# Performance work log

Measured on AMD Instinct MI355X. Metric: run time of the kernel, lower is better.

The kernel has to match this reference:

```python
import jax, jax.numpy as jnp
import numpy as np

N = 50000      # nodes
DEG = 16       # in-degree per node -> E = 800k edges
IN = 256       # in_size
HID = 32       # hid_size
HEAD = 4       # heads in first layer
OUT = 40       # out_size (classes)
HH = HID * HEAD  # 128, hidden width
NEG_SLOPE = 0.2


def setup_inputs() -> dict:
    key = jax.random.key(0)
    ks = jax.random.split(key, 16)
    E = N * DEG
    src = jax.random.randint(ks[0], (E,), 0, N)
    dst = jnp.repeat(jnp.arange(N), DEG)  # every node has DEG in-edges

    def nrm(k, shape):
        return jax.random.normal(k, shape, jnp.float32) * 0.1

    return dict(
        features=jax.random.normal(ks[1], (N, IN), jnp.float32),
        src=src, dst=dst,
        # layer 1: GATConv(IN -> HID, HEAD heads)
        W1=nrm(ks[2], (IN, HH)), al1=nrm(ks[3], (HEAD, HID)), ar1=nrm(ks[4], (HEAD, HID)), b1=nrm(ks[5], (HH,)),
        # hidden layer: GATConv(HH -> HH, 1 head)
        Wh=nrm(ks[6], (HH, HH)), alh=nrm(ks[7], (1, HH)), arh=nrm(ks[8], (1, HH)), bh=nrm(ks[9], (HH,)),
        # layer 2: GATConv(HH -> OUT, 1 head)
        W2=nrm(ks[10], (HH, OUT)), al2=nrm(ks[11], (1, OUT)), ar2=nrm(ks[12], (1, OUT)), b2=nrm(ks[13], (OUT,)),
    )


def gat_conv(x, src, dst, W, al, ar, b):
    """DGL-style GATConv. x:[N,F], W:[F,H*D], al/ar:[H,D], b:[H*D]. Returns [N,H,D]."""
    n = x.shape[0]
    H, D = al.shape
    feat = (x @ W).reshape(n, H, D)                 # [N,H,D]
    el = jnp.sum(feat * al, axis=-1)                # [N,H]
    er = jnp.sum(feat * ar, axis=-1)                # [N,H]
    e = jax.nn.leaky_relu(el[src] + er[dst], NEG_SLOPE)  # [E,H] per-edge logits
    # segment softmax over each destination's in-edges
    emax = jax.lax.stop_gradient(jax.ops.segment_max(e, dst, num_segments=n))  # [N,H]
    ex = jnp.exp(e - emax[dst])                     # [E,H]
    den = jax.ops.segment_sum(ex, dst, num_segments=n)  # [N,H]
    alpha = ex / den[dst]                           # [E,H]
    out = jax.ops.segment_sum(feat[src] * alpha[:, :, None], dst, num_segments=n)  # [N,H,D]
    return out + b.reshape(1, H, D)


def reference(features, src, dst, W1, al1, ar1, b1, Wh, alh, arh, bh, W2, al2, ar2, b2):
    # conv1 -> flatten heads -> relu
    h = jax.nn.relu(gat_conv(features, src, dst, W1, al1, ar1, b1).reshape(N, HH))
    # hidden GATConv (1 head) -> mean over head -> relu (dropout is identity in eval)
    h = jax.nn.relu(gat_conv(h, src, dst, Wh, alh, arh, bh).mean(axis=1))
    # conv2 (1 head) -> mean over head -> log_softmax
    h = gat_conv(h, src, dst, W2, al2, ar2, b2).mean(axis=1)
    return jax.nn.log_softmax(h, axis=1)
```

## Files before the change

### kernel.cpp

```cpp
#include <hip/hip_runtime.h>
#include <cstddef>
#include <math.h>

#define NN 50000
#define DEG 16
#define NEG_SLOPE 0.2f

typedef __attribute__((ext_vector_type(8))) short bf16x8;
typedef __attribute__((ext_vector_type(4))) float f32x4;

__device__ inline unsigned short f2bf(float x) {
    unsigned u = __float_as_uint(x);
    return (unsigned short)((u + 0x7FFF + ((u >> 16) & 1)) >> 16);
}
__device__ inline float bf2f(unsigned short u) {
    return __uint_as_float(((unsigned)u) << 16);
}
__device__ inline unsigned pack_bf2(float lo, float hi) {
    return (unsigned)f2bf(lo) | ((unsigned)f2bf(hi) << 16);
}
__device__ inline void gld_lds16f(const float* g, float* l) {
    __builtin_amdgcn_global_load_lds((const __attribute__((address_space(1))) void*)g,
                                     (__attribute__((address_space(3))) void*)l, 16, 0, 0);
}

__global__ void prep_k(const float* __restrict__ W1, unsigned short* __restrict__ Wt1,
                       const float* __restrict__ Wh, unsigned short* __restrict__ Wth,
                       const float* __restrict__ W2, unsigned short* __restrict__ W2t)
{
    const int b = blockIdx.x;
    if (b < 128) {
        int idx = b * 256 + threadIdx.x;
        int c = idx >> 8, k = idx & 255;
        Wt1[idx] = f2bf(W1[(size_t)k * 128 + c]);
    } else if (b < 192) {
        int idx = (b - 128) * 256 + threadIdx.x;
        int c = idx >> 7, k = idx & 127;
        Wth[idx] = f2bf(Wh[(size_t)k * 128 + c]);
    } else {
        int idx = (b - 192) * 256 + threadIdx.x;
        if (idx < 48 * 128) {
            int c = idx >> 7, k = idx & 127;
            W2t[idx] = (c < 40) ? f2bf(W2[(size_t)k * 40 + c]) : (unsigned short)0;
        }
    }
}

__launch_bounds__(256)
__global__ void gemm1_k(const float* __restrict__ A,
                        const unsigned short* __restrict__ Wt,
                        const float* __restrict__ al, const float* __restrict__ ar,
                        unsigned short* __restrict__ feat,
                        float* __restrict__ el, float* __restrict__ er)
{
    constexpr int K = 256, KS = 8, TPB = 2;
    __shared__ __align__(16) float buf[2][4096];
    const int tid = threadIdx.x;
    const int w = tid >> 6, l = tid & 63;
    const int lr = l & 15, lq = l >> 4;
    const int col0 = w * 32;

    bf16x8 B0[KS], B1[KS];
#pragma unroll
    for (int ks = 0; ks < KS; ks++) {
        B0[ks] = *(const bf16x8*)(Wt + (size_t)(col0 + lr) * K + ks * 32 + lq * 8);
        B1[ks] = *(const bf16x8*)(Wt + (size_t)(col0 + 16 + lr) * K + ks * 32 + lq * 8);
    }

    const int t0 = blockIdx.x * TPB;
    const int tmax = NN / 16;
    const int t1 = (t0 + TPB < tmax) ? t0 + TPB : tmax;
    if (t0 >= tmax) return;

    auto stage = [&](int t, int b) {
#pragma unroll
        for (int p = 0; p < 4; p++) {
            int j = tid + p * 256;
            int row = j >> 6;
            int kg = (j & 63) ^ (row & 7);
            gld_lds16f(A + (size_t)(t * 16 + row) * 256 + kg * 4, &buf[b][(size_t)j * 4]);
        }
    };
    stage(t0, t0 & 1);

    for (int t = t0; t < t1; ++t) {
        __syncthreads();
        if (t + 1 < t1) stage(t + 1, (t + 1) & 1);

        f32x4 acc0 = {0.f, 0.f, 0.f, 0.f}, acc1 = {0.f, 0.f, 0.f, 0.f};
        const float* bb = buf[t & 1];
#pragma unroll
        for (int ks = 0; ks < KS; ks++) {
            const int kg0 = ks * 8 + lq * 2;
            const int s0 = lr * 64 + (kg0 ^ (lr & 7));
            const int s1 = lr * 64 + ((kg0 + 1) ^ (lr & 7));
            float4 va = *(const float4*)&bb[(size_t)s0 * 4];
            float4 vb = *(const float4*)&bb[(size_t)s1 * 4];
            bf16x8 a = {(short)f2bf(va.x), (short)f2bf(va.y),
                        (short)f2bf(va.z), (short)f2bf(va.w),
                        (short)f2bf(vb.x), (short)f2bf(vb.y),
                        (short)f2bf(vb.z), (short)f2bf(vb.w)};
            acc0 = __builtin_amdgcn_mfma_f32_16x16x32_bf16(a, B0[ks], acc0, 0, 0, 0);
            acc1 = __builtin_amdgcn_mfma_f32_16x16x32_bf16(a, B1[ks], acc1, 0, 0, 0);
        }

        const int row0 = t * 16;
#pragma unroll
        for (int reg = 0; reg < 4; reg++) {
            const int r = row0 + lq * 4 + reg;
            feat[(size_t)r * 128 + col0 + lr]      = f2bf(acc0[reg]);
            feat[(size_t)r * 128 + col0 + 16 + lr] = f2bf(acc1[reg]);
        }

        float pe[4], pr[4];
#pragma unroll
        for (int reg = 0; reg < 4; reg++) {
            pe[reg] = acc0[reg] * al[col0 + lr] + acc1[reg] * al[col0 + 16 + lr];
            pr[reg] = acc0[reg] * ar[col0 + lr] + acc1[reg] * ar[col0 + 16 + lr];
        }
#pragma unroll
        for (int m = 1; m < 16; m <<= 1)
#pragma unroll
            for (int reg = 0; reg < 4; reg++) {
                pe[reg] += __shfl_xor(pe[reg], m);
                pr[reg] += __shfl_xor(pr[reg], m);
            }
        if (lr == 0) {
#pragma unroll
            for (int reg = 0; reg < 4; reg++) {
                const int r = row0 + lq * 4 + reg;
                el[r * 4 + w] = pe[reg];
                er[r * 4 + w] = pr[reg];
            }
        }
    }
}

__launch_bounds__(256)
__global__ void fusedh_k(const unsigned short* __restrict__ feat1,
                         const float* __restrict__ el1, const float* __restrict__ er1,
                         const int* __restrict__ src, const float* __restrict__ b1,
                         const unsigned short* __restrict__ Wt,
                         const float* __restrict__ alh, const float* __restrict__ arh,
                         unsigned short* __restrict__ feat2,
                         float* __restrict__ el, float* __restrict__ er)
{
    __shared__ __align__(16) unsigned short abuf[256 * 8];
    __shared__ float s_alpha[16][64];
    __shared__ float redE[4][16], redR[4][16];
    const int tid = threadIdx.x;
    const int w = tid >> 6, lane = tid & 63;
    const int q = lane >> 4, li = lane & 15;
    const int slot = w * 4 + q;
    const int row0 = blockIdx.x * 16;
    const int node = row0 + slot;
    const int col0 = w * 32;

    const int s = src[node * DEG + li];
    {
        const float4 elv = *(const float4*)(el1 + (size_t)s * 4);
        const float4 erv = *(const float4*)(er1 + (size_t)node * 4);
        float e[4] = {elv.x + erv.x, elv.y + erv.y, elv.z + erv.z, elv.w + erv.w};
#pragma unroll
        for (int h = 0; h < 4; h++) {
            float x = e[h];
            x = (x > 0.f) ? x : NEG_SLOPE * x;
            float mx = x;
#pragma unroll
            for (int d = 1; d < 16; d <<= 1) mx = fmaxf(mx, __shfl_xor(mx, d, 16));
            float ex = expf(x - mx);
            float den = ex;
#pragma unroll
            for (int d = 1; d < 16; d <<= 1) den += __shfl_xor(den, d, 16);
            s_alpha[slot][h * 16 + li] = ex / den;
        }
    }
    uint4 v[16];
#pragma unroll
    for (int jj = 0; jj < 16; jj++) {
        int sj = __shfl(s, (lane & 48) | jj);
        v[jj] = *(const uint4*)(feat1 + (size_t)sj * 128 + li * 8);
    }
    float acc[8] = {0.f, 0.f, 0.f, 0.f, 0.f, 0.f, 0.f, 0.f};
    const int hrow = (li >> 2) * 16;
#pragma unroll
    for (int jj = 0; jj < 16; jj++) {
        float a = s_alpha[slot][hrow + jj];
        unsigned u0 = v[jj].x, u1 = v[jj].y, u2 = v[jj].z, u3 = v[jj].w;
        acc[0] += a * bf2f((unsigned short)(u0 & 0xFFFF));
        acc[1] += a * bf2f((unsigned short)(u0 >> 16));
        acc[2] += a * bf2f((unsigned short)(u1 & 0xFFFF));
        acc[3] += a * bf2f((unsigned short)(u1 >> 16));
        acc[4] += a * bf2f((unsigned short)(u2 & 0xFFFF));
        acc[5] += a * bf2f((unsigned short)(u2 >> 16));
        acc[6] += a * bf2f((unsigned short)(u3 & 0xFFFF));
        acc[7] += a * bf2f((unsigned short)(u3 >> 16));
    }
    const float4 bb0 = *(const float4*)(b1 + li * 8);
    const float4 bb1 = *(const float4*)(b1 + li * 8 + 4);
    float o[8];
    o[0] = fmaxf(acc[0] + bb0.x, 0.f); o[1] = fmaxf(acc[1] + bb0.y, 0.f);
    o[2] = fmaxf(acc[2] + bb0.z, 0.f); o[3] = fmaxf(acc[3] + bb0.w, 0.f);
    o[4] = fmaxf(acc[4] + bb1.x, 0.f); o[5] = fmaxf(acc[5] + bb1.y, 0.f);
    o[6] = fmaxf(acc[6] + bb1.z, 0.f); o[7] = fmaxf(acc[7] + bb1.w, 0.f);
    {
        uint4 pk;
        pk.x = pack_bf2(o[0], o[1]);
        pk.y = pack_bf2(o[2], o[3]);
        pk.z = pack_bf2(o[4], o[5]);
        pk.w = pack_bf2(o[6], o[7]);
        int jw = ((li >> 2) * 64 + (li & 3) * 16 + slot) ^ (li & 7);
        *(uint4*)&abuf[(size_t)jw * 8] = pk;
    }

    bf16x8 B0[4], B1[4];
#pragma unroll
    for (int ks = 0; ks < 4; ks++) {
        B0[ks] = *(const bf16x8*)(Wt + (size_t)(col0 + li) * 128 + ks * 32 + q * 8);
        B1[ks] = *(const bf16x8*)(Wt + (size_t)(col0 + 16 + li) * 128 + ks * 32 + q * 8);
    }
    __syncthreads();

    f32x4 acc0 = {0.f, 0.f, 0.f, 0.f}, acc1 = {0.f, 0.f, 0.f, 0.f};
#pragma unroll
    for (int ks = 0; ks < 4; ks++) {
        int jr = (ks * 64 + lane) ^ ((ks * 4 + q) & 7);
        bf16x8 a = *(const bf16x8*)&abuf[(size_t)jr * 8];
        acc0 = __builtin_amdgcn_mfma_f32_16x16x32_bf16(a, B0[ks], acc0, 0, 0, 0);
        acc1 = __builtin_amdgcn_mfma_f32_16x16x32_bf16(a, B1[ks], acc1, 0, 0, 0);
    }

#pragma unroll
    for (int reg = 0; reg < 4; reg++) {
        const int r = row0 + q * 4 + reg;
        feat2[(size_t)r * 128 + col0 + li]      = f2bf(acc0[reg]);
        feat2[(size_t)r * 128 + col0 + 16 + li] = f2bf(acc1[reg]);
    }
    float pe[4], pr[4];
#pragma unroll
    for (int reg = 0; reg < 4; reg++) {
        pe[reg] = acc0[reg] * alh[col0 + li] + acc1[reg] * alh[col0 + 16 + li];
        pr[reg] = acc0[reg] * arh[col0 + li] + acc1[reg] * arh[col0 + 16 + li];
    }
#pragma unroll
    for (int m = 1; m < 16; m <<= 1)
#pragma unroll
        for (int reg = 0; reg < 4; reg++) {
            pe[reg] += __shfl_xor(pe[reg], m);
            pr[reg] += __shfl_xor(pr[reg], m);
        }
    if (li == 0) {
#pragma unroll
        for (int reg = 0; reg < 4; reg++) {
            redE[w][q * 4 + reg] = pe[reg];
            redR[w][q * 4 + reg] = pr[reg];
        }
    }
    __syncthreads();
    if (tid < 16) {
        el[row0 + tid] = redE[0][tid] + redE[1][tid] + redE[2][tid] + redE[3][tid];
        er[row0 + tid] = redR[0][tid] + redR[1][tid] + redR[2][tid] + redR[3][tid];
    }
}

__launch_bounds__(256)
__global__ void fused40_k(const unsigned short* __restrict__ feat2,
                          const float* __restrict__ elA, const float* __restrict__ erA,
                          const int* __restrict__ src, const float* __restrict__ bh,
                          const unsigned short* __restrict__ W2t,
                          const float* __restrict__ al2, const float* __restrict__ ar2,
                          unsigned short* __restrict__ f40,
                          float* __restrict__ el2, float* __restrict__ er2)
{
    __shared__ __align__(16) unsigned short abuf[512 * 8];
    __shared__ float redE[4][16], redR[4][16];
    const int tid = threadIdx.x;
    const int w = tid >> 6, lane = tid & 63;
    const int q = lane >> 4, li = lane & 15;
    const int slot = w * 4 + q;
    const int row0 = blockIdx.x * 32;

#pragma unroll
    for (int rnd = 0; rnd < 2; rnd++) {
        const int row = rnd * 16 + slot;
        int node = row0 + row;
        if (node > NN - 1) node = NN - 1;
        const int s = src[node * DEG + li];
        float x = elA[s] + erA[node];
        x = (x > 0.f) ? x : NEG_SLOPE * x;
        float mx = x;
#pragma unroll
        for (int d = 1; d < 16; d <<= 1) mx = fmaxf(mx, __shfl_xor(mx, d, 16));
        float ex = expf(x - mx);
        float den = ex;
#pragma unroll
        for (int d = 1; d < 16; d <<= 1) den += __shfl_xor(den, d, 16);
        const float alpha = ex / den;

        uint4 v[16];
#pragma unroll
        for (int jj = 0; jj < 16; jj++) {
            int sj = __shfl(s, (lane & 48) | jj);
            v[jj] = *(const uint4*)(feat2 + (size_t)sj * 128 + li * 8);
        }
        float acc[8] = {0.f, 0.f, 0.f, 0.f, 0.f, 0.f, 0.f, 0.f};
#pragma unroll
        for (int jj = 0; jj < 16; jj++) {
            float a = __shfl(alpha, (lane & 48) | jj);
            unsigned u0 = v[jj].x, u1 = v[jj].y, u2 = v[jj].z, u3 = v[jj].w;
            acc[0] += a * bf2f((unsigned short)(u0 & 0xFFFF));
            acc[1] += a * bf2f((unsigned short)(u0 >> 16));
            acc[2] += a * bf2f((unsigned short)(u1 & 0xFFFF));
            acc[3] += a * bf2f((unsigned short)(u1 >> 16));
            acc[4] += a * bf2f((unsigned short)(u2 & 0xFFFF));
            acc[5] += a * bf2f((unsigned short)(u2 >> 16));
            acc[6] += a * bf2f((unsigned short)(u3 & 0xFFFF));
            acc[7] += a * bf2f((unsigned short)(u3 >> 16));
        }
        const float4 bb0 = *(const float4*)(bh + li * 8);
        const float4 bb1 = *(const float4*)(bh + li * 8 + 4);
        float o[8];
        o[0] = fmaxf(acc[0] + bb0.x, 0.f); o[1] = fmaxf(acc[1] + bb0.y, 0.f);
        o[2] = fmaxf(acc[2] + bb0.z, 0.f); o[3] = fmaxf(acc[3] + bb0.w, 0.f);
        o[4] = fmaxf(acc[4] + bb1.x, 0.f); o[5] = fmaxf(acc[5] + bb1.y, 0.f);
        o[6] = fmaxf(acc[6] + bb1.z, 0.f); o[7] = fmaxf(acc[7] + bb1.w, 0.f);
        uint4 pk;
        pk.x = pack_bf2(o[0], o[1]);
        pk.y = pack_bf2(o[2], o[3]);
        pk.z = pack_bf2(o[4], o[5]);
        pk.w = pack_bf2(o[6], o[7]);
        int jw = rnd * 256 + li * 16 + (slot ^ (li & 7));
        *(uint4*)&abuf[(size_t)jw * 8] = pk;
    }

    const int rw = w & 1, cw = w >> 1;
    const int cf0 = cw ? 2 : 0, cf1 = cw ? 2 : 1;
    bf16x8 Bf0[4], Bf1[4];
#pragma unroll
    for (int ks = 0; ks < 4; ks++) {
        Bf0[ks] = *(const bf16x8*)(W2t + (size_t)(cf0 * 16 + li) * 128 + ks * 32 + q * 8);
        Bf1[ks] = *(const bf16x8*)(W2t + (size_t)(cf1 * 16 + li) * 128 + ks * 32 + q * 8);
    }
    __syncthreads();

    f32x4 acc0 = {0.f, 0.f, 0.f, 0.f}, acc1 = {0.f, 0.f, 0.f, 0.f};
#pragma unroll
    for (int ks = 0; ks < 4; ks++) {
        const int kg = ks * 4 + q;
        const int jr = rw * 256 + kg * 16 + (li ^ (kg & 7));
        bf16x8 a = *(const bf16x8*)&abuf[(size_t)jr * 8];
        acc0 = __builtin_amdgcn_mfma_f32_16x16x32_bf16(a, Bf0[ks], acc0, 0, 0, 0);
        acc1 = __builtin_amdgcn_mfma_f32_16x16x32_bf16(a, Bf1[ks], acc1, 0, 0, 0);
    }

    const int col0v = cf0 * 16 + li, col1v = cf1 * 16 + li;
#pragma unroll
    for (int reg = 0; reg < 4; reg++) {
        const int r = row0 + rw * 16 + q * 4 + reg;
        if (r < NN) {
            if (col0v < 40) f40[(size_t)r * 40 + col0v] = f2bf(acc0[reg]);
            if (cw == 0)    f40[(size_t)r * 40 + col1v] = f2bf(acc1[reg]);
        }
    }
    const float a20 = (col0v < 40) ? al2[col0v] : 0.f;
    const float r20 = (col0v < 40) ? ar2[col0v] : 0.f;
    const float a21 = (cw == 0) ? al2[col1v] : 0.f;
    const float r21 = (cw == 0) ? ar2[col1v] : 0.f;
    float pe[4], pr[4];
#pragma unroll
    for (int reg = 0; reg < 4; reg++) {
        pe[reg] = acc0[reg] * a20 + acc1[reg] * a21;
        pr[reg] = acc0[reg] * r20 + acc1[reg] * r21;
    }
#pragma unroll
    for (int m = 1; m < 16; m <<= 1)
#pragma unroll
        for (int reg = 0; reg < 4; reg++) {
            pe[reg] += __shfl_xor(pe[reg], m);
            pr[reg] += __shfl_xor(pr[reg], m);
        }
    if (li == 0) {
#pragma unroll
        for (int reg = 0; reg < 4; reg++) {
            redE[w][q * 4 + reg] = pe[reg];
            redR[w][q * 4 + reg] = pr[reg];
        }
    }
    __syncthreads();
    if (tid < 32) {
        const int rwi = tid >> 4, idx = tid & 15;
        const int r = row0 + rwi * 16 + idx;
        if (r < NN) {
            el2[r] = redE[rwi][idx] + redE[rwi + 2][idx];
            er2[r] = redR[rwi][idx] + redR[rwi + 2][idx];
        }
    }
}

__launch_bounds__(256)
__global__ void agg40_ls_k(const unsigned short* __restrict__ feat, const float* __restrict__ el,
                           const float* __restrict__ er, const int* __restrict__ src,
                           const float* __restrict__ bias, float* __restrict__ out)
{
    const int tid = threadIdx.x;
    const int w = tid >> 6, lane = tid & 63;
    const int half = lane >> 5, li = lane & 31;
    const int node = blockIdx.x * 8 + w * 2 + half;

    const int s = src[node * DEG + (li & 15)];
    float e = el[s] + er[node];
    e = (e > 0.f) ? e : NEG_SLOPE * e;
    float mx = e;
#pragma unroll
    for (int d = 1; d < 16; d <<= 1) mx = fmaxf(mx, __shfl_xor(mx, d, 16));
    float ex = expf(e - mx);
    float den = ex;
#pragma unroll
    for (int d = 1; d < 16; d <<= 1) den += __shfl_xor(den, d, 16);
    const float alpha = ex / den;

    const int cli = (li < 20) ? li : 19;
    float acc0 = 0.f, acc1 = 0.f;
#pragma unroll
    for (int jj = 0; jj < DEG; jj++) {
        int sj = __shfl(s, jj, 32);
        float a = __shfl(alpha, jj, 32);
        unsigned v = *(const unsigned*)(feat + (size_t)sj * 40 + 2 * cli);
        acc0 += a * bf2f((unsigned short)(v & 0xFFFF));
        acc1 += a * bf2f((unsigned short)(v >> 16));
    }
    float v0 = acc0 + bias[2 * cli], v1 = acc1 + bias[2 * cli + 1];
    float m2 = (li < 20) ? fmaxf(v0, v1) : -INFINITY;
#pragma unroll
    for (int d = 1; d < 32; d <<= 1) m2 = fmaxf(m2, __shfl_xor(m2, d, 32));
    float pe = (li < 20) ? (expf(v0 - m2) + expf(v1 - m2)) : 0.f;
    float se = pe;
#pragma unroll
    for (int d = 1; d < 32; d <<= 1) se += __shfl_xor(se, d, 32);
    if (li < 20) {
        float ls = m2 + logf(se);
        out[(size_t)node * 40 + 2 * li]     = v0 - ls;
        out[(size_t)node * 40 + 2 * li + 1] = v1 - ls;
    }
}

extern "C" void kernel_launch(void* const* d_in, const int* in_sizes, int n_in,
                              void* d_out, int out_size, void* d_ws, size_t ws_size,
                              hipStream_t stream)
{
    const float* features = (const float*)d_in[0];
    const int*   src      = (const int*)d_in[1];
    const float* W1  = (const float*)d_in[3];
    const float* al1 = (const float*)d_in[4];
    const float* ar1 = (const float*)d_in[5];
    const float* b1  = (const float*)d_in[6];
    const float* Wh  = (const float*)d_in[7];
    const float* alh = (const float*)d_in[8];
    const float* arh = (const float*)d_in[9];
    const float* bh  = (const float*)d_in[10];
    const float* W2  = (const float*)d_in[11];
    const float* al2 = (const float*)d_in[12];
    const float* ar2 = (const float*)d_in[13];
    const float* b2  = (const float*)d_in[14];
    float* out = (float*)d_out;

    float* ws = (float*)d_ws;
    unsigned short* featb  = (unsigned short*)ws;
    unsigned short* featb2 = featb + (size_t)NN * 128;
    float* el1  = (float*)(featb2 + (size_t)NN * 128);
    float* er1  = el1 + (size_t)NN * 4;
    float* elA  = er1 + (size_t)NN * 4;
    float* erA  = elA + NN;
    float* el2  = erA + NN;
    float* er2  = el2 + NN;
    unsigned short* f40b = (unsigned short*)(er2 + NN);
    unsigned short* Wt1  = f40b + (size_t)NN * 40;
    unsigned short* Wth  = Wt1 + 128 * 256;
    unsigned short* W2t  = Wth + 128 * 128;

    dim3 blk(256);
    prep_k<<<216, blk, 0, stream>>>(W1, Wt1, Wh, Wth, W2, W2t);
    gemm1_k<<<1563, blk, 0, stream>>>(features, Wt1, al1, ar1, featb, el1, er1);
    fusedh_k<<<3125, blk, 0, stream>>>(featb, el1, er1, src, b1, Wth, alh, arh,
                                       featb2, elA, erA);
    fused40_k<<<1563, blk, 0, stream>>>(featb2, elA, erA, src, bh, W2t, al2, ar2,
                                        f40b, el2, er2);
    agg40_ls_k<<<6250, blk, 0, stream>>>(f40b, el2, er2, src, b2, out);
}
```

Measured before the change: 114.1 us.

## Prefetch both GEMM tiles upfront and issue gathers before softmax

In gemm1_k, both A tiles of the block are issued to LDS at the start. Explicit vmcnt waits and barriers let the first tile be computed while the second is still loading, and the loop becomes straight-line compute/epilogue code. In the two gather kernels, the neighbour feature loads are moved ahead of the edge-softmax math so that their memory latency overlaps the exp and shuffle reductions. The hand-written vmcnt counts depend on the exact number of outstanding loads, which is fragile, and the early gathers raise register pressure.

```diff
diff --git a/kernel.cpp b/kernel.cpp
--- a/kernel.cpp
+++ b/kernel.cpp
@@ -60,17 +60,17 @@
     const int lr = l & 15, lq = l >> 4;
     const int col0 = w * 32;
 
+    const int t0 = blockIdx.x * TPB;
+    const int tmax = NN / 16;
+    if (t0 >= tmax) return;
+    const bool two = (t0 + 1 < tmax);
+
     bf16x8 B0[KS], B1[KS];
 #pragma unroll
     for (int ks = 0; ks < KS; ks++) {
         B0[ks] = *(const bf16x8*)(Wt + (size_t)(col0 + lr) * K + ks * 32 + lq * 8);
         B1[ks] = *(const bf16x8*)(Wt + (size_t)(col0 + 16 + lr) * K + ks * 32 + lq * 8);
     }
-
-    const int t0 = blockIdx.x * TPB;
-    const int tmax = NN / 16;
-    const int t1 = (t0 + TPB < tmax) ? t0 + TPB : tmax;
-    if (t0 >= tmax) return;
 
     auto stage = [&](int t, int b) {
 #pragma unroll
@@ -81,13 +81,15 @@
             gld_lds16f(A + (size_t)(t * 16 + row) * 256 + kg * 4, &buf[b][(size_t)j * 4]);
         }
     };
-    stage(t0, t0 & 1);
-
-    for (int t = t0; t < t1; ++t) {
-        __syncthreads();
-        if (t + 1 < t1) stage(t + 1, (t + 1) & 1);
-
-        f32x4 acc0 = {0.f, 0.f, 0.f, 0.f}, acc1 = {0.f, 0.f, 0.f, 0.f};
+    stage(t0, 0);
+    if (two) stage(t0 + 1, 1);
+
+    if (two) { asm volatile("s_waitcnt vmcnt(4)" ::: "memory"); }
+    else     { asm volatile("s_waitcnt vmcnt(0)" ::: "memory"); }
+    __builtin_amdgcn_sched_barrier(0);
+    __builtin_amdgcn_s_barrier();
+
+    auto compute = [&](int t, f32x4& a0, f32x4& a1) {
         const float* bb = buf[t & 1];
 #pragma unroll
         for (int ks = 0; ks < KS; ks++) {
@@ -100,10 +102,11 @@
                         (short)f2bf(va.z), (short)f2bf(va.w),
                         (short)f2bf(vb.x), (short)f2bf(vb.y),
                         (short)f2bf(vb.z), (short)f2bf(vb.w)};
-            acc0 = __builtin_amdgcn_mfma_f32_16x16x32_bf16(a, B0[ks], acc0, 0, 0, 0);
-            acc1 = __builtin_amdgcn_mfma_f32_16x16x32_bf16(a, B1[ks], acc1, 0, 0, 0);
-        }
-
+            a0 = __builtin_amdgcn_mfma_f32_16x16x32_bf16(a, B0[ks], a0, 0, 0, 0);
+            a1 = __builtin_amdgcn_mfma_f32_16x16x32_bf16(a, B1[ks], a1, 0, 0, 0);
+        }
+    };
+    auto epilogue = [&](int t, const f32x4& acc0, const f32x4& acc1) {
         const int row0 = t * 16;
 #pragma unroll
         for (int reg = 0; reg < 4; reg++) {
@@ -111,7 +114,6 @@
             feat[(size_t)r * 128 + col0 + lr]      = f2bf(acc0[reg]);
             feat[(size_t)r * 128 + col0 + 16 + lr] = f2bf(acc1[reg]);
         }
-
         float pe[4], pr[4];
 #pragma unroll
         for (int reg = 0; reg < 4; reg++) {
@@ -133,6 +135,20 @@
                 er[r * 4 + w] = pr[reg];
             }
         }
+    };
+
+    f32x4 a00 = {0.f, 0.f, 0.f, 0.f}, a01 = {0.f, 0.f, 0.f, 0.f};
+    compute(t0, a00, a01);
+    if (two) {
+        asm volatile("s_waitcnt vmcnt(0)" ::: "memory");
+        __builtin_amdgcn_sched_barrier(0);
+        __builtin_amdgcn_s_barrier();
+    }
+    epilogue(t0, a00, a01);
+    if (two) {
+        f32x4 a10 = {0.f, 0.f, 0.f, 0.f}, a11 = {0.f, 0.f, 0.f, 0.f};
+        compute(t0 + 1, a10, a11);
+        epilogue(t0 + 1, a10, a11);
     }
 }
 
@@ -157,6 +173,14 @@
     const int col0 = w * 32;
 
     const int s = src[node * DEG + li];
+
+    uint4 v[16];
+#pragma unroll
+    for (int jj = 0; jj < 16; jj++) {
+        int sj = __shfl(s, (lane & 48) | jj);
+        v[jj] = *(const uint4*)(feat1 + (size_t)sj * 128 + li * 8);
+    }
+
     {
         const float4 elv = *(const float4*)(el1 + (size_t)s * 4);
         const float4 erv = *(const float4*)(er1 + (size_t)node * 4);
@@ -175,12 +199,7 @@
             s_alpha[slot][h * 16 + li] = ex / den;
         }
     }
-    uint4 v[16];
-#pragma unroll
-    for (int jj = 0; jj < 16; jj++) {
-        int sj = __shfl(s, (lane & 48) | jj);
-        v[jj] = *(const uint4*)(feat1 + (size_t)sj * 128 + li * 8);
-    }
+
     float acc[8] = {0.f, 0.f, 0.f, 0.f, 0.f, 0.f, 0.f, 0.f};
     const int hrow = (li >> 2) * 16;
 #pragma unroll
@@ -286,6 +305,14 @@
         int node = row0 + row;
         if (node > NN - 1) node = NN - 1;
         const int s = src[node * DEG + li];
+
+        uint4 v[16];
+#pragma unroll
+        for (int jj = 0; jj < 16; jj++) {
+            int sj = __shfl(s, (lane & 48) | jj);
+            v[jj] = *(const uint4*)(feat2 + (size_t)sj * 128 + li * 8);
+        }
+
         float x = elA[s] + erA[node];
         x = (x > 0.f) ? x : NEG_SLOPE * x;
         float mx = x;
@@ -297,12 +324,6 @@
         for (int d = 1; d < 16; d <<= 1) den += __shfl_xor(den, d, 16);
         const float alpha = ex / den;
 
-        uint4 v[16];
-#pragma unroll
-        for (int jj = 0; jj < 16; jj++) {
-            int sj = __shfl(s, (lane & 48) | jj);
-            v[jj] = *(const uint4*)(feat2 + (size_t)sj * 128 + li * 8);
-        }
         float acc[8] = {0.f, 0.f, 0.f, 0.f, 0.f, 0.f, 0.f, 0.f};
 #pragma unroll
         for (int jj = 0; jj < 16; jj++) {
```

Measured after the change: 113.4 us. Within noise of the previous version (-0.6%).
